# Kernel optimization log

Measured on AMD Instinct MI355X. Metric: run time of the kernel, lower is better.

The kernel has to match this reference:

```python
import jax, jax.numpy as jnp
import numpy as np

N, M = 100000, 800000
F_IN, F_E, H = 64, 16, 64
T_NODE, T_EDGE = 2, 3
HEAD_DIM = 16.0


def setup_inputs() -> dict:
    key = jax.random.key(0)
    ks = jax.random.split(key, 16)
    inp = {
        "x": jax.random.normal(ks[0], (N, F_IN), jnp.float32),
        "edge_feat": jax.random.normal(ks[1], (M, F_E), jnp.float32),
        "node_type": jax.random.randint(ks[2], (N,), 0, T_NODE, jnp.int32),
        "edge_src": jax.random.randint(ks[3], (M,), 0, N, jnp.int32),
        "edge_dst": jax.random.randint(ks[4], (M,), 0, N, jnp.int32),
        "edge_type": jax.random.randint(ks[5], (M,), 0, T_EDGE, jnp.int32),
    }
    s_n = 1.0 / np.sqrt(F_IN)
    s_e = 1.0 / np.sqrt(F_E)
    for i, name in enumerate(["W1", "W2", "W3", "W4"]):
        inp[name] = jax.random.normal(ks[6 + i], (T_NODE, F_IN, H), jnp.float32) * s_n
        inp["b" + name[1]] = jax.random.normal(ks[10 + i], (T_NODE, H), jnp.float32) * 0.01
    inp["W5"] = jax.random.normal(ks[14], (T_EDGE, F_E, H), jnp.float32) * s_e
    inp["b5"] = jax.random.normal(ks[15], (T_EDGE, H), jnp.float32) * 0.01
    return inp


def _node_proj(x, W, b, node_type):
    # per-node-type linear: [T,F,H] weights, select row per node type
    p = jnp.einsum('nf,tfh->tnh', x, W) + b[:, None, :]      # [T,N,H]
    return jnp.take_along_axis(p, node_type[None, :, None], axis=0)[0]  # [N,H]


def reference(x, edge_feat, W1, b1, W2, b2, W3, b3, W4, b4, W5, b5,
              node_type, edge_src, edge_dst, edge_type):
    n = x.shape[0]
    h1 = _node_proj(x, W1, b1, node_type)
    h2 = _node_proj(x, W2, b2, node_type)
    h3 = _node_proj(x, W3, b3, node_type)
    h4 = _node_proj(x, W4, b4, node_type)
    # per-edge-type linear via weight gather (F_E is small)
    w5e = jnp.einsum('mf,mfh->mh', edge_feat, W5[edge_type]) + b5[edge_type]  # [M,H]
    # scalar attention logit per edge (w3_i . (w4_j + w5_ij)) / sqrt(head_dim)
    num = jnp.sum(h3[edge_dst] * (h4[edge_src] + w5e), axis=-1)  # [M]
    # softmax over a single scalar per edge == 1.0 exactly (faithful to source)
    score = jax.nn.softmax((num / jnp.sqrt(HEAD_DIM))[:, None], axis=-1)[:, 0]  # [M]
    msg = score[:, None] * (h2[edge_src] + w5e)                  # [M,H]
    out = h1 + jax.ops.segment_sum(msg, edge_dst, num_segments=n)
    return out
```

## Files before the change

### kernel.cpp

```cpp
#include <hip/hip_runtime.h>


#define CAP 16
#define OVF_CAP 32768

typedef __attribute__((ext_vector_type(8))) short short8;
typedef __attribute__((ext_vector_type(4))) float f32x4;

__device__ __forceinline__ float b2f(unsigned short u) {
    union { unsigned v; float f; } x; x.v = ((unsigned)u) << 16; return x.f;
}
__device__ __forceinline__ unsigned short f2b(float f) {
    union { float f; unsigned v; } x; x.f = f;
    unsigned u = x.v;
    unsigned r = (u + 0x7FFFu + ((u >> 16) & 1u)) >> 16;
    return (unsigned short)r;
}

__global__ __launch_bounds__(256) void k1_gemm_scatter(
    const float* __restrict__ x, const int* __restrict__ nt,
    const float* __restrict__ W1, const float* __restrict__ b1,
    const float* __restrict__ W2, const float* __restrict__ b2,
    const int* __restrict__ esrc, const int* __restrict__ edst,
    const int* __restrict__ etype,
    int* __restrict__ cnt32, int* __restrict__ ovfCnt,
    int4* __restrict__ ovf, int2* __restrict__ rec,
    float* __restrict__ out, unsigned short* __restrict__ h2b,
    int N, int M)
{
    __shared__ __align__(16) unsigned short sx[128 * 72];
    __shared__ __align__(16) unsigned short sw[4][64 * 72];
    __shared__ int snt[128];

    int tid = threadIdx.x;

    if (blockIdx.x & 1) {
        int e0 = (blockIdx.x >> 1) * 1024 + tid;
        int dd[4], ssrc[4], tty[4];
        bool v[4];
#pragma unroll
        for (int j = 0; j < 4; ++j) {
            int e = e0 + j * 256;
            v[j] = e < M;
            int ec = v[j] ? e : 0;
            dd[j]   = edst[ec];
            ssrc[j] = esrc[ec];
            tty[j]  = etype[ec];
        }
        int pos[4];
#pragma unroll
        for (int j = 0; j < 4; ++j)
            if (v[j]) pos[j] = atomicAdd(&cnt32[dd[j]], 1);
#pragma unroll
        for (int j = 0; j < 4; ++j) {
            if (!v[j]) continue;
            int packed = ssrc[j] | (tty[j] << 20);
            int e = e0 + j * 256;
            if (pos[j] < CAP) {
                rec[dd[j] * CAP + pos[j]] = make_int2(packed, e);
            } else {
                int slot = atomicAdd(ovfCnt, 1);
                if (slot < OVF_CAP) ovf[slot] = make_int4(packed, e, dd[j], 0);
            }
        }
        return;
    }

    int rowbase = (blockIdx.x >> 1) * 128;

    const float* Wm0 = W1;
    const float* Wm1 = W1 + 4096;
    const float* Wm2 = W2;
    const float* Wm3 = W2 + 4096;
#pragma unroll
    for (int j = 0; j < 4; ++j) {
        int k  = (tid >> 4) + j * 16;
        int n4 = (tid & 15) * 4;
        float4 w0 = *(const float4*)&Wm0[k * 64 + n4];
        float4 w1v = *(const float4*)&Wm1[k * 64 + n4];
        float4 w2v = *(const float4*)&Wm2[k * 64 + n4];
        float4 w3 = *(const float4*)&Wm3[k * 64 + n4];
        sw[0][(n4 + 0) * 72 + k] = f2b(w0.x);
        sw[0][(n4 + 1) * 72 + k] = f2b(w0.y);
        sw[0][(n4 + 2) * 72 + k] = f2b(w0.z);
        sw[0][(n4 + 3) * 72 + k] = f2b(w0.w);
        sw[1][(n4 + 0) * 72 + k] = f2b(w1v.x);
        sw[1][(n4 + 1) * 72 + k] = f2b(w1v.y);
        sw[1][(n4 + 2) * 72 + k] = f2b(w1v.z);
        sw[1][(n4 + 3) * 72 + k] = f2b(w1v.w);
        sw[2][(n4 + 0) * 72 + k] = f2b(w2v.x);
        sw[2][(n4 + 1) * 72 + k] = f2b(w2v.y);
        sw[2][(n4 + 2) * 72 + k] = f2b(w2v.z);
        sw[2][(n4 + 3) * 72 + k] = f2b(w2v.w);
        sw[3][(n4 + 0) * 72 + k] = f2b(w3.x);
        sw[3][(n4 + 1) * 72 + k] = f2b(w3.y);
        sw[3][(n4 + 2) * 72 + k] = f2b(w3.z);
        sw[3][(n4 + 3) * 72 + k] = f2b(w3.w);
    }

    if (tid < 128) {
        int r = rowbase + tid;
        snt[tid] = (r < N) ? nt[r] : 0;
    }

    int fr = (tid & 15) * 4;
    int ir = tid >> 4;
#pragma unroll
    for (int it = 0; it < 8; ++it) {
        int i = it * 16 + ir;
        int r = rowbase + i;
        float4 v = make_float4(0.f, 0.f, 0.f, 0.f);
        if (r < N) v = *(const float4*)&x[(size_t)r * 64 + fr];
        ushort4 p;
        p.x = f2b(v.x); p.y = f2b(v.y); p.z = f2b(v.z); p.w = f2b(v.w);
        *(ushort4*)&sx[i * 72 + fr] = p;
    }
    __syncthreads();

    int lane = tid & 63;
    int wid  = tid >> 6;
    int q    = lane >> 4;
    int cc   = lane & 15;
    int m0   = wid * 32;

    f32x4 acc[4][2][4];
#pragma unroll
    for (int mm = 0; mm < 4; ++mm)
#pragma unroll
        for (int s = 0; s < 2; ++s)
#pragma unroll
            for (int t = 0; t < 4; ++t)
                acc[mm][s][t] = (f32x4){0.f, 0.f, 0.f, 0.f};

#pragma unroll
    for (int k0 = 0; k0 < 64; k0 += 32) {
        int ko = k0 + q * 8;
        short8 af0 = *(short8*)&sx[(m0 + cc) * 72 + ko];
        short8 af1 = *(short8*)&sx[(m0 + 16 + cc) * 72 + ko];
#pragma unroll
        for (int mm = 0; mm < 4; ++mm)
#pragma unroll
            for (int t = 0; t < 4; ++t) {
                short8 bf = *(short8*)&sw[mm][(t * 16 + cc) * 72 + ko];
                acc[mm][0][t] = __builtin_amdgcn_mfma_f32_16x16x32_bf16(
                    af0, bf, acc[mm][0][t], 0, 0, 0);
                acc[mm][1][t] = __builtin_amdgcn_mfma_f32_16x16x32_bf16(
                    af1, bf, acc[mm][1][t], 0, 0, 0);
            }
    }

    float b1v[2][4], b2v[2][4];
#pragma unroll
    for (int ty = 0; ty < 2; ++ty)
#pragma unroll
        for (int t = 0; t < 4; ++t) {
            b1v[ty][t] = b1[ty * 64 + t * 16 + cc];
            b2v[ty][t] = b2[ty * 64 + t * 16 + cc];
        }

#pragma unroll
    for (int s = 0; s < 2; ++s)
#pragma unroll
        for (int reg = 0; reg < 4; ++reg) {
            int rl = m0 + s * 16 + q * 4 + reg;
            int r = rowbase + rl;
            if (r < N) {
                int ty = snt[rl];
#pragma unroll
                for (int t = 0; t < 4; ++t) {
                    float v1 = (ty ? acc[1][s][t][reg] : acc[0][s][t][reg])
                               + b1v[ty][t];
                    float v2 = (ty ? acc[3][s][t][reg] : acc[2][s][t][reg])
                               + b2v[ty][t];
                    out[(size_t)r * 64 + t * 16 + cc] = v1;
                    h2b[(size_t)r * 64 + t * 16 + cc] = f2b(v2);
                }
            }
        }
}

__global__ __launch_bounds__(256) void k2_gather(
    const float* __restrict__ ef, const int2* __restrict__ rec,
    const int* __restrict__ cnt32,
    const float* __restrict__ W5, const float* __restrict__ b5,
    const int4* __restrict__ ovf, const int* __restrict__ ovfCnt,
    const unsigned short* __restrict__ h2b, float* __restrict__ out,
    int N, int gatherBlocks, int ovfBlocks)
{
    __shared__ float sW[3072 + 192];
    __shared__ float sG[4][64];

    int tid = threadIdx.x;
    for (int k = tid; k < 816; k += 256) {
        ((float4*)sW)[k] = (k < 768) ? ((const float4*)W5)[k]
                                     : ((const float4*)b5)[k - 768];
    }
    __syncthreads();

    int lane = tid & 63;
    int wid = tid >> 6;

    if (blockIdx.x >= (unsigned)gatherBlocks) {
        int novf = min(*ovfCnt, OVF_CAP);
        int gw = (blockIdx.x - gatherBlocks) * 4 + wid;
        int nw = ovfBlocks * 4;
        for (int ri = gw; ri < novf; ri += nw) {
            int4 o = ovf[ri];
            int s = o.x & 0xFFFFF;
            int t = (unsigned)o.x >> 20;
            float acc = sW[3072 + t * 64 + lane] +
                        b2f(h2b[(size_t)s * 64 + lane]);
#pragma unroll
            for (int f = 0; f < 16; ++f)
                acc = fmaf(ef[(size_t)o.y * 16 + f],
                           sW[(t * 16 + f) * 64 + lane], acc);
            unsafeAtomicAdd(&out[(size_t)o.z * 64 + lane], acc);
        }
        return;
    }

    int d = blockIdx.x * 4 + wid;
    bool active = d < N;
    int deg = 0;
    if (active) deg = min(cnt32[d], CAP);
    int base = d * CAP;

    int myt = (lane < 48) ? (lane >> 4) : (lane - 48);
    int myf = lane & 15;
    float accH = 0.f, accS = 0.f;

    for (int i = 0; i < deg; i += 8) {
        int nrem = deg - i;
        int2 r[8];
#pragma unroll
        for (int j = 0; j < 8; ++j) {
            int ij = i + j;
            ij = (ij < deg) ? ij : (deg - 1);
            r[j] = rec[base + ij];
        }
        float hv[8], ev[8];
#pragma unroll
        for (int j = 0; j < 8; ++j) {
            int s = r[j].x & 0xFFFFF;
            hv[j] = b2f(h2b[(size_t)s * 64 + lane]);
            ev[j] = ef[(size_t)r[j].y * 16 + myf];
        }
#pragma unroll
        for (int j = 0; j < 8; ++j) {
            int t = (unsigned)r[j].x >> 20;
            bool ok = j < nrem;
            accH += ok ? hv[j] : 0.f;
            float v = (lane < 48) ? ev[j] : 1.0f;
            accS += (ok && (t == myt)) ? v : 0.f;
        }
    }

    sG[wid][lane] = accS;
    float rr = accH;
    const float* g = sG[wid];
#pragma unroll
    for (int j = 0; j < 48; ++j)
        rr = fmaf(g[j], sW[j * 64 + lane], rr);
#pragma unroll
    for (int t = 0; t < 3; ++t)
        rr = fmaf(g[48 + t], sW[3072 + t * 64 + lane], rr);

    if (active)
        unsafeAtomicAdd(&out[(size_t)d * 64 + lane], rr);
}

extern "C" void kernel_launch(void* const* d_in, const int* in_sizes, int n_in,
                              void* d_out, int out_size, void* d_ws, size_t ws_size,
                              hipStream_t stream) {
    const float* x  = (const float*)d_in[0];
    const float* ef = (const float*)d_in[1];
    const int* nt   = (const int*)d_in[2];
    const int* es   = (const int*)d_in[3];
    const int* ed   = (const int*)d_in[4];
    const int* et   = (const int*)d_in[5];
    const float* W1 = (const float*)d_in[6];
    const float* b1 = (const float*)d_in[7];
    const float* W2 = (const float*)d_in[8];
    const float* b2 = (const float*)d_in[9];
    const float* W5 = (const float*)d_in[14];
    const float* b5 = (const float*)d_in[15];

    int N = in_sizes[2];
    int M = in_sizes[3];

    char* w = (char*)d_ws;
    size_t off = 0;
    unsigned short* h2b = (unsigned short*)(w + off); off += (size_t)N * 64 * 2;
    off = (off + 255) & ~(size_t)255;
    int2* rec = (int2*)(w + off); off += (size_t)N * CAP * 8;
    off = (off + 255) & ~(size_t)255;
    int4* ovf = (int4*)(w + off); off += (size_t)OVF_CAP * 16;
    off = (off + 255) & ~(size_t)255;
    int* ovfCnt = (int*)(w + off);
    int* cnt32  = (int*)(w + off + 64);
    size_t zeroBytes = 64 + (size_t)N * 4;

    float* out = (float*)d_out;

    hipMemsetAsync(ovfCnt, 0, zeroBytes, stream);

    int gemmBlocks    = (N + 127) / 128;
    int scatterBlocks = (M + 1023) / 1024;
    int gb1 = 2 * max(gemmBlocks, scatterBlocks);
    k1_gemm_scatter<<<gb1, 256, 0, stream>>>(
        x, nt, W1, b1, W2, b2, es, ed, et,
        cnt32, ovfCnt, ovf, rec, out, h2b, N, M);

    int gatherBlocks = (N + 3) / 4;
    int ovfBlocks = 32;
    k2_gather<<<gatherBlocks + ovfBlocks, 256, 0, stream>>>(
        ef, rec, cnt32, W5, b5, ovf, ovfCnt, h2b, out,
        N, gatherBlocks, ovfBlocks);
}
```

Measured before the change: 303.1 us.

## Process multiple nodes per wave in gather with prefetched records and register weights

New measurement: 361.0 us. 19.1% more time.

```diff
diff --git a/kernel.cpp b/kernel.cpp
--- a/kernel.cpp
+++ b/kernel.cpp
@@ -3,6 +3,7 @@
 
 #define CAP 16
 #define OVF_CAP 32768
+#define GPW 8
 
 typedef __attribute__((ext_vector_type(8))) short short8;
 typedef __attribute__((ext_vector_type(4))) float f32x4;
@@ -15,6 +16,12 @@
     unsigned u = x.v;
     unsigned r = (u + 0x7FFFu + ((u >> 16) & 1u)) >> 16;
     return (unsigned short)r;
+}
+__device__ __forceinline__ float rl(float v, int j) {
+    union { float f; int i; } a, b;
+    a.f = v;
+    b.i = __builtin_amdgcn_readlane(a.i, j);
+    return b.f;
 }
 
 __global__ __launch_bounds__(256) void k1_gemm_scatter(
@@ -162,10 +169,10 @@
     for (int s = 0; s < 2; ++s)
 #pragma unroll
         for (int reg = 0; reg < 4; ++reg) {
-            int rl = m0 + s * 16 + q * 4 + reg;
-            int r = rowbase + rl;
+            int rl_ = m0 + s * 16 + q * 4 + reg;
+            int r = rowbase + rl_;
             if (r < N) {
-                int ty = snt[rl];
+                int ty = snt[rl_];
 #pragma unroll
                 for (int t = 0; t < 4; ++t) {
                     float v1 = (ty ? acc[1][s][t][reg] : acc[0][s][t][reg])
@@ -179,7 +186,7 @@
         }
 }
 
-__global__ __launch_bounds__(256) void k2_gather(
+__global__ __launch_bounds__(256, 3) void k2_gather(
     const float* __restrict__ ef, const int2* __restrict__ rec,
     const int* __restrict__ cnt32,
     const float* __restrict__ W5, const float* __restrict__ b5,
@@ -187,16 +194,7 @@
     const unsigned short* __restrict__ h2b, float* __restrict__ out,
     int N, int gatherBlocks, int ovfBlocks)
 {
-    __shared__ float sW[3072 + 192];
-    __shared__ float sG[4][64];
-
     int tid = threadIdx.x;
-    for (int k = tid; k < 816; k += 256) {
-        ((float4*)sW)[k] = (k < 768) ? ((const float4*)W5)[k]
-                                     : ((const float4*)b5)[k - 768];
-    }
-    __syncthreads();
-
     int lane = tid & 63;
     int wid = tid >> 6;
 
@@ -208,65 +206,101 @@
             int4 o = ovf[ri];
             int s = o.x & 0xFFFFF;
             int t = (unsigned)o.x >> 20;
-            float acc = sW[3072 + t * 64 + lane] +
-                        b2f(h2b[(size_t)s * 64 + lane]);
+            float acc = b5[t * 64 + lane] + b2f(h2b[((size_t)s << 6) | lane]);
 #pragma unroll
             for (int f = 0; f < 16; ++f)
                 acc = fmaf(ef[(size_t)o.y * 16 + f],
-                           sW[(t * 16 + f) * 64 + lane], acc);
+                           W5[(t * 16 + f) * 64 + lane], acc);
             unsafeAtomicAdd(&out[(size_t)o.z * 64 + lane], acc);
         }
         return;
     }
 
-    int d = blockIdx.x * 4 + wid;
-    bool active = d < N;
-    int deg = 0;
-    if (active) deg = min(cnt32[d], CAP);
-    int base = d * CAP;
-
+    float Wcol[51];
+#pragma unroll
+    for (int j = 0; j < 48; ++j) Wcol[j] = W5[j * 64 + lane];
+#pragma unroll
+    for (int t = 0; t < 3; ++t) Wcol[48 + t] = b5[t * 64 + lane];
+
+    int base_d = (blockIdx.x * 4 + wid) * GPW;
     int myt = (lane < 48) ? (lane >> 4) : (lane - 48);
-    int myf = lane & 15;
-    float accH = 0.f, accS = 0.f;
-
-    for (int i = 0; i < deg; i += 8) {
-        int nrem = deg - i;
-        int2 r[8];
-#pragma unroll
-        for (int j = 0; j < 8; ++j) {
-            int ij = i + j;
-            ij = (ij < deg) ? ij : (deg - 1);
-            r[j] = rec[base + ij];
-        }
-        float hv[8], ev[8];
-#pragma unroll
-        for (int j = 0; j < 8; ++j) {
-            int s = r[j].x & 0xFFFFF;
-            hv[j] = b2f(h2b[(size_t)s * 64 + lane]);
-            ev[j] = ef[(size_t)r[j].y * 16 + myf];
-        }
-#pragma unroll
-        for (int j = 0; j < 8; ++j) {
-            int t = (unsigned)r[j].x >> 20;
-            bool ok = j < nrem;
-            accH += ok ? hv[j] : 0.f;
-            float v = (lane < 48) ? ev[j] : 1.0f;
-            accS += (ok && (t == myt)) ? v : 0.f;
-        }
-    }
-
-    sG[wid][lane] = accS;
-    float rr = accH;
-    const float* g = sG[wid];
-#pragma unroll
-    for (int j = 0; j < 48; ++j)
-        rr = fmaf(g[j], sW[j * 64 + lane], rr);
-#pragma unroll
-    for (int t = 0; t < 3; ++t)
-        rr = fmaf(g[48 + t], sW[3072 + t * 64 + lane], rr);
-
-    if (active)
-        unsafeAtomicAdd(&out[(size_t)d * 64 + lane], rr);
+    unsigned myf = lane & 15;
+    bool fl = lane < 48;
+
+    int degC = 0;
+    int2 rC[8];
+    if (base_d < N) {
+        degC = cnt32[base_d];
+        unsigned rb = (unsigned)base_d * CAP;
+#pragma unroll
+        for (int j = 0; j < 8; ++j) rC[j] = rec[rb + j];
+    }
+
+#pragma unroll 1
+    for (int g = 0; g < GPW; ++g) {
+        int d = base_d + g;
+        int dn = d + 1;
+        int degN = 0;
+        int2 rN[8];
+        if (g + 1 < GPW && dn < N) {
+            degN = cnt32[dn];
+            unsigned rb = (unsigned)dn * CAP;
+#pragma unroll
+            for (int j = 0; j < 8; ++j) rN[j] = rec[rb + j];
+        }
+
+        if (d < N) {
+            int dg = min(degC, CAP);
+            if (dg > 0) {
+                float accH = 0.f, accS = 0.f;
+#pragma unroll
+                for (int j = 0; j < 8; ++j) {
+                    bool ok = j < dg;
+                    int px = ok ? rC[j].x : 0;
+                    int py = ok ? rC[j].y : 0;
+                    unsigned s = (unsigned)px & 0xFFFFFu;
+                    float hv = b2f(h2b[((size_t)s << 6) | (unsigned)lane]);
+                    float evv = ef[((unsigned)py << 4) | myf];
+                    int t = (int)((unsigned)px >> 20);
+                    accH += ok ? hv : 0.f;
+                    float v = fl ? evv : 1.0f;
+                    accS += (ok && t == myt) ? v : 0.f;
+                }
+                if (dg > 8) {
+                    int dgm1 = dg - 1;
+                    unsigned rb = (unsigned)d * CAP;
+                    int2 r2[8];
+#pragma unroll
+                    for (int j = 0; j < 8; ++j)
+                        r2[j] = rec[rb + (unsigned)min(8 + j, dgm1)];
+#pragma unroll
+                    for (int j = 0; j < 8; ++j) {
+                        unsigned s = (unsigned)r2[j].x & 0xFFFFFu;
+                        float hv = b2f(h2b[((size_t)s << 6) | (unsigned)lane]);
+                        float evv = ef[((unsigned)r2[j].y << 4) | myf];
+                        int t = (int)((unsigned)r2[j].x >> 20);
+                        bool ok = (8 + j) < dg;
+                        accH += ok ? hv : 0.f;
+                        float v = fl ? evv : 1.0f;
+                        accS += (ok && t == myt) ? v : 0.f;
+                    }
+                }
+                float rr0 = accH, rr1 = 0.f, rr2 = 0.f;
+#pragma unroll
+                for (int j = 0; j < 17; ++j) {
+                    rr0 = fmaf(rl(accS, 3 * j + 0), Wcol[3 * j + 0], rr0);
+                    rr1 = fmaf(rl(accS, 3 * j + 1), Wcol[3 * j + 1], rr1);
+                    rr2 = fmaf(rl(accS, 3 * j + 2), Wcol[3 * j + 2], rr2);
+                }
+                float rr = rr0 + (rr1 + rr2);
+                unsafeAtomicAdd(&out[((size_t)(unsigned)d << 6) | lane], rr);
+            }
+        }
+
+        degC = degN;
+#pragma unroll
+        for (int j = 0; j < 8; ++j) rC[j] = rN[j];
+    }
 }
 
 extern "C" void kernel_launch(void* const* d_in, const int* in_sizes, int n_in,
@@ -311,7 +345,7 @@
         x, nt, W1, b1, W2, b2, es, ed, et,
         cnt32, ovfCnt, ovf, rec, out, h2b, N, M);
 
-    int gatherBlocks = (N + 3) / 4;
+    int gatherBlocks = (N + 4 * GPW - 1) / (4 * GPW);
     int ovfBlocks = 32;
     k2_gather<<<gatherBlocks + ovfBlocks, 256, 0, stream>>>(
         ef, rec, cnt32, W5, b5, ovf, ovfCnt, h2b, out,
```
